# Kernel optimization log

Measured on AMD Instinct MI355X. Metric: run time of the kernel, lower is better.

The kernel has to match this reference:

```python
import jax, jax.numpy as jnp
import numpy as np

EMBED_DIM = 1024
NUM_HEADS = 16
HEAD_DIM = EMBED_DIM // NUM_HEADS


def setup_inputs() -> dict:
    key = jax.random.key(0)
    k1, k2, k3, k4, k5 = jax.random.split(key, 5)
    B, T, C = 2, 2048, EMBED_DIM
    s = 1.0 / np.sqrt(C)
    return {
        "x": jax.random.normal(k1, (B, T, C), dtype=jnp.float32),
        "W_qkv": jax.random.normal(k2, (C, 3 * C), dtype=jnp.float32) * s,
        "b_qkv": jnp.zeros((3 * C,), dtype=jnp.float32),
        "W_out": jax.random.normal(k3, (C, C), dtype=jnp.float32) * s,
        "b_out": jnp.zeros((C,), dtype=jnp.float32),
    }


def reference(x, W_qkv, b_qkv, W_out, b_out):
    B, T, C = x.shape
    H, D = NUM_HEADS, HEAD_DIM
    qkv = x @ W_qkv + b_qkv                       # [B, T, 3C]
    q, k, v = jnp.split(qkv, 3, axis=-1)
    # [B, H, T, D]
    q = q.reshape(B, T, H, D).transpose(0, 2, 1, 3)
    k = k.reshape(B, T, H, D).transpose(0, 2, 1, 3)
    v = v.reshape(B, T, H, D).transpose(0, 2, 1, 3)
    scores = jnp.einsum("bhqd,bhkd->bhqk", q, k) / np.sqrt(D)  # [B,H,T,T]
    causal = jnp.tril(jnp.ones((T, T), dtype=bool))
    scores = jnp.where(causal[None, None], scores, -jnp.inf)
    weights = jax.nn.softmax(scores, axis=-1)
    out = jnp.einsum("bhqk,bhkd->bhqd", weights, v)  # [B,H,T,D]
    out = out.transpose(0, 2, 1, 3).reshape(B, T, C)
    return out @ W_out + b_out
```

## Files before the change

### kernel.cpp

```cpp
#include <hip/hip_runtime.h>
#include <stdint.h>

typedef unsigned short u16t;
typedef __attribute__((ext_vector_type(8))) short bf16x8;
typedef __attribute__((ext_vector_type(4))) float f32x4;

#define DEV __device__ __forceinline__

DEV u16t f2bf(float f) {
  union { float f; unsigned u; } v; v.f = f;
  unsigned r = v.u + 0x7FFFu + ((v.u >> 16) & 1u);
  return (u16t)(r >> 16);
}

DEV unsigned cvtpk(float a, float b) {
  unsigned r;
  asm("v_cvt_pk_bf16_f32 %0, %1, %2" : "=v"(r) : "v"(a), "v"(b));
  return r;
}

DEV void glds16(const void* g, void* l) {
  __builtin_amdgcn_global_load_lds((const __attribute__((address_space(1))) void*)g,
                                   (__attribute__((address_space(3))) void*)l, 16, 0, 0);
}

__global__ __launch_bounds__(256) void k_cast_x(const float* __restrict__ x,
                                                u16t* __restrict__ xb, int n) {
  int i = (blockIdx.x * 256 + threadIdx.x) * 8;
  if (i >= n) return;
  const float4* p = (const float4*)(x + i);
  float4 a = p[0], b = p[1];
  union { u16t h[8]; int4 v; } o;
  o.h[0] = f2bf(a.x); o.h[1] = f2bf(a.y); o.h[2] = f2bf(a.z); o.h[3] = f2bf(a.w);
  o.h[4] = f2bf(b.x); o.h[5] = f2bf(b.y); o.h[6] = f2bf(b.z); o.h[7] = f2bf(b.w);
  *(int4*)(xb + i) = o.v;
}

__global__ __launch_bounds__(256) void k_transpose_cast(const float* __restrict__ src,
                                                        u16t* __restrict__ dst,
                                                        int R, int C) {
  __shared__ u16t tile[64][65];
  int c0 = blockIdx.x * 64, r0 = blockIdx.y * 64;
  int tid = threadIdx.x;
#pragma unroll
  for (int i = 0; i < 16; i++) {
    int idx = tid + i * 256;
    int r = idx >> 6, c = idx & 63;
    tile[c][r] = f2bf(src[(size_t)(r0 + r) * C + (c0 + c)]);
  }
  __syncthreads();
#pragma unroll
  for (int i = 0; i < 16; i++) {
    int idx = tid + i * 256;
    int rr = idx >> 6, cc = idx & 63;
    dst[(size_t)(c0 + rr) * R + (r0 + cc)] = tile[rr][cc];
  }
}

template <int K>
DEV void gemm_mainloop(const u16t* __restrict__ A, const u16t* __restrict__ Bt,
                       int m0, int n0, u16t* ldsA, u16t* ldsB, f32x4 acc[4][4]) {
  const int tid = threadIdx.x;
  const int lane = tid & 63;
  const int wid = tid >> 6;
  const int wm = wid >> 1, wn = wid & 1;
#pragma unroll
  for (int i = 0; i < 4; i++)
#pragma unroll
    for (int j = 0; j < 4; j++) acc[i][j] = f32x4{0.f, 0.f, 0.f, 0.f};

  char* lA = (char*)ldsA;
  char* lB = (char*)ldsB;

  for (int k0 = 0; k0 < K; k0 += 32) {
#pragma unroll
    for (int j = 0; j < 2; j++) {
      int g = wid * 64 + lane + j * 256;
      int row = g >> 2;
      int cb = (g & 3) * 16;
      glds16((const char*)(A + (size_t)(m0 + row) * K + k0) + cb,
             lA + j * 4096 + wid * 1024);
      glds16((const char*)(Bt + (size_t)(n0 + row) * K + k0) + cb,
             lB + j * 4096 + wid * 1024);
    }
    __syncthreads();
    bf16x8 af[4], bfr[4];
    const int lr = lane & 15;
    const int ko = (lane >> 4) * 8;
#pragma unroll
    for (int f = 0; f < 4; f++) {
      af[f]  = *(const bf16x8*)(ldsA + (wm * 64 + f * 16 + lr) * 32 + ko);
      bfr[f] = *(const bf16x8*)(ldsB + (wn * 64 + f * 16 + lr) * 32 + ko);
    }
#pragma unroll
    for (int i = 0; i < 4; i++)
#pragma unroll
      for (int j = 0; j < 4; j++)
        acc[i][j] = __builtin_amdgcn_mfma_f32_16x16x32_bf16(af[i], bfr[j], acc[i][j], 0, 0, 0);
    __syncthreads();
  }
}

__global__ __launch_bounds__(256) void k_gemm_qkv(const u16t* __restrict__ xb,
                                                  const u16t* __restrict__ wt,
                                                  const float* __restrict__ bias,
                                                  u16t* __restrict__ q,
                                                  u16t* __restrict__ kk,
                                                  u16t* __restrict__ vt) {
  __shared__ u16t ldsA[128 * 32];
  __shared__ u16t ldsB[128 * 32];
  __shared__ u16t ldsE[4][64 * 64];
  const int m0 = blockIdx.x * 128, n0 = blockIdx.y * 128;
  f32x4 acc[4][4];
  gemm_mainloop<1024>(xb, wt, m0, n0, ldsA, ldsB, acc);

  const int lane = threadIdx.x & 63, wid = threadIdx.x >> 6;
  const int wm = wid >> 1, wn = wid & 1;
  const int nbase = n0 + wn * 64;
  const int which = nbase >> 10;
  const int hb = (nbase & 1023) >> 6;
  const int bb = m0 >> 11;
  const int t0 = (m0 & 2047) + wm * 64;
  const int bh = bb * 16 + hb;
  u16t* eb = ldsE[wid];
#pragma unroll
  for (int fm = 0; fm < 4; fm++) {
#pragma unroll
    for (int fn = 0; fn < 4; fn++) {
      float bv = bias[nbase + fn * 16 + (lane & 15)];
#pragma unroll
      for (int i = 0; i < 4; i++) {
        int t_loc = fm * 16 + (lane >> 4) * 4 + i;
        int d_loc = fn * 16 + (lane & 15);
        float v = acc[fm][fn][i] + bv;
        if (which == 2) eb[d_loc * 64 + t_loc] = f2bf(v);
        else            eb[t_loc * 64 + d_loc] = f2bf(v);
      }
    }
  }
  asm volatile("s_waitcnt lgkmcnt(0)" ::: "memory");
  u16t* dst;
  size_t base, rowstride;
  if (which == 2) { dst = vt; base = (size_t)bh * 64 * 2048 + t0; rowstride = 2048; }
  else { dst = (which == 0) ? q : kk; base = ((size_t)bh * 2048 + t0) * 64; rowstride = 64; }
#pragma unroll
  for (int it = 0; it < 8; it++) {
    int g = it * 64 + lane;
    int r = g >> 3;
    int ce = (g & 7) * 8;
    *(int4*)(dst + base + (size_t)r * rowstride + ce) = *(const int4*)(eb + r * 64 + ce);
  }
}

__global__ __launch_bounds__(128) void k_attn(const u16t* __restrict__ q,
                                              const u16t* __restrict__ kk,
                                              const u16t* __restrict__ vt,
                                              u16t* __restrict__ attn) {
  __shared__ u16t ldsK[2][64 * 64];
  __shared__ u16t ldsV[2][64 * 64];
  __shared__ u16t ldsP[2][16 * 64];
  const int p = blockIdx.x;
  const int t_lo = p, t_hi = 63 - p;
  const int lo_tiles = (t_lo >> 1) + 1;
  const int hi_tiles = (t_hi >> 1) + 1;
  const int bh = blockIdx.y;
  const int tid = threadIdx.x;
  const int lane = tid & 63, wid = tid >> 6;
  const int lr = lane & 15, lg = lane >> 4;
  const size_t hbase = (size_t)bh * 2048 * 64;
  const size_t vbase = (size_t)bh * 64 * 2048;
  const float NINF = -__builtin_inff();
  const float CEXP = 0.1803368801111204f;

  bf16x8 qlo[2], qhi[2];
  {
    const u16t* qp  = q + hbase + (size_t)(t_lo * 32 + wid * 16 + lr) * 64 + lg * 8;
    const u16t* qp2 = q + hbase + (size_t)(t_hi * 32 + wid * 16 + lr) * 64 + lg * 8;
#pragma unroll
    for (int ks = 0; ks < 2; ks++) {
      qlo[ks] = *(const bf16x8*)(qp + ks * 32);
      qhi[ks] = *(const bf16x8*)(qp2 + ks * 32);
    }
  }

  f32x4 olo[4], ohi[4];
#pragma unroll
  for (int i = 0; i < 4; i++) {
    olo[i] = f32x4{0.f, 0.f, 0.f, 0.f};
    ohi[i] = f32x4{0.f, 0.f, 0.f, 0.f};
  }
  float mlo = NINF, llo = 0.f, mhi = NINF, lhi = 0.f;

  u16t* pb = ldsP[wid];

  auto stage = [&](int buf, int kt) {
#pragma unroll
    for (int j = 0; j < 4; j++) {
      int g = j * 128 + tid;
      int r = g >> 3;
      int cb = (g & 7) * 16;
      int sc = cb ^ ((r & 7) << 4);
      glds16((const char*)(kk + hbase + (size_t)(kt * 64 + r) * 64) + sc,
             (char*)ldsK[buf] + j * 2048 + wid * 1024);
      glds16((const char*)(vt + vbase + (size_t)r * 2048 + kt * 64) + sc,
             (char*)ldsV[buf] + j * 2048 + wid * 1024);
    }
  };

  auto compute = [&](int buf, bool diag, int moff, const bf16x8* qf, f32x4* o,
                     float& m_run, float& l_run) {
    const char* K = (const char*)ldsK[buf];
    const char* V = (const char*)ldsV[buf];
    float sv[4][4];
    __builtin_amdgcn_s_setprio(1);
#pragma unroll
    for (int f = 0; f < 4; f++) {
      f32x4 s = f32x4{0.f, 0.f, 0.f, 0.f};
#pragma unroll
      for (int ks = 0; ks < 2; ks++) {
        int row = f * 16 + lr;
        int cb = ks * 64 + lg * 16;
        bf16x8 kf = *(const bf16x8*)(K + row * 128 + (cb ^ ((row & 7) << 4)));
        s = __builtin_amdgcn_mfma_f32_16x16x32_bf16(kf, qf[ks], s, 0, 0, 0);
      }
#pragma unroll
      for (int i = 0; i < 4; i++) sv[f][i] = s[i];
    }
    __builtin_amdgcn_s_setprio(0);
    if (diag) {
      int qr = moff + wid * 16 + lr;
#pragma unroll
      for (int f = 0; f < 4; f++)
#pragma unroll
        for (int i = 0; i < 4; i++)
          if (f * 16 + lg * 4 + i > qr) sv[f][i] = NINF;
    }
    float m0a = fmaxf(fmaxf(sv[0][0], sv[0][1]), fmaxf(sv[0][2], sv[0][3]));
    float m1a = fmaxf(fmaxf(sv[1][0], sv[1][1]), fmaxf(sv[1][2], sv[1][3]));
    float m2a = fmaxf(fmaxf(sv[2][0], sv[2][1]), fmaxf(sv[2][2], sv[2][3]));
    float m3a = fmaxf(fmaxf(sv[3][0], sv[3][1]), fmaxf(sv[3][2], sv[3][3]));
    float mx = fmaxf(fmaxf(m0a, m1a), fmaxf(m2a, m3a));
    mx = fmaxf(mx, __shfl_xor(mx, 16));
    mx = fmaxf(mx, __shfl_xor(mx, 32));
    if (!__all(mx <= m_run + 8.0f)) {
      float mnew = fmaxf(m_run, mx);
      float al = exp2f((m_run - mnew) * CEXP);
      m_run = mnew;
      l_run *= al;
#pragma unroll
      for (int df = 0; df < 4; df++)
#pragma unroll
        for (int i = 0; i < 4; i++) o[df][i] *= al;
    }
    const float nmc = -m_run * CEXP;
    float ps[4][4];
    float fs[4];
#pragma unroll
    for (int f = 0; f < 4; f++) {
#pragma unroll
      for (int i = 0; i < 4; i++)
        ps[f][i] = exp2f(__builtin_fmaf(sv[f][i], CEXP, nmc));
      fs[f] = (ps[f][0] + ps[f][1]) + (ps[f][2] + ps[f][3]);
    }
    float ssum = (fs[0] + fs[1]) + (fs[2] + fs[3]);
    ssum += __shfl_xor(ssum, 16);
    ssum += __shfl_xor(ssum, 32);
    l_run += ssum;
#pragma unroll
    for (int f = 0; f < 4; f++) {
      union { unsigned u[2]; uint2 v; } pk;
      pk.u[0] = cvtpk(ps[f][0], ps[f][1]);
      pk.u[1] = cvtpk(ps[f][2], ps[f][3]);
      int cby = (f * 32 + lg * 8) ^ ((lr & 7) << 4);
      *(uint2*)((char*)pb + lr * 128 + cby) = pk.v;
    }
    asm volatile("s_waitcnt lgkmcnt(0)" ::: "memory");
    __builtin_amdgcn_s_setprio(1);
#pragma unroll
    for (int ks = 0; ks < 2; ks++) {
      int cb = ks * 64 + lg * 16;
      bf16x8 pf = *(const bf16x8*)((const char*)pb + lr * 128 + (cb ^ ((lr & 7) << 4)));
#pragma unroll
      for (int df = 0; df < 4; df++) {
        int vrow = df * 16 + lr;
        bf16x8 vf = *(const bf16x8*)(V + vrow * 128 + (cb ^ ((vrow & 7) << 4)));
        o[df] = __builtin_amdgcn_mfma_f32_16x16x32_bf16(vf, pf, o[df], 0, 0, 0);
      }
    }
    __builtin_amdgcn_s_setprio(0);
  };

  stage(0, 0);
  __syncthreads();
  for (int kt = 0; kt < hi_tiles; kt++) {
    int cur = kt & 1;
    if (kt + 1 < hi_tiles) stage(cur ^ 1, kt + 1);
    compute(cur, kt == (t_hi >> 1), (t_hi & 1) << 5, qhi, ohi, mhi, lhi);
    if (kt < lo_tiles) compute(cur, kt == (t_lo >> 1), (t_lo & 1) << 5, qlo, olo, mlo, llo);
    __syncthreads();
  }

  const int bb = bh >> 4, h = bh & 15;
  auto epi = [&](int qt, const f32x4* o, float l_run) {
    float rinv = 1.0f / l_run;
    int t = qt * 32 + wid * 16 + lr;
    size_t rowb = ((size_t)bb * 2048 + t) * 1024 + h * 64;
#pragma unroll
    for (int df = 0; df < 4; df++) {
      union { unsigned u[2]; uint2 v; } pk;
      pk.u[0] = cvtpk(o[df][0] * rinv, o[df][1] * rinv);
      pk.u[1] = cvtpk(o[df][2] * rinv, o[df][3] * rinv);
      *(uint2*)(attn + rowb + df * 16 + lg * 4) = pk.v;
    }
  };
  epi(t_lo, olo, llo);
  epi(t_hi, ohi, lhi);
}

__global__ __launch_bounds__(256) void k_gemm_out(const u16t* __restrict__ attn,
                                                  const u16t* __restrict__ wt,
                                                  const float* __restrict__ bias,
                                                  float* __restrict__ out) {
  __shared__ u16t ldsA[128 * 32];
  __shared__ u16t ldsB[128 * 32];
  const int m0 = blockIdx.x * 128, n0 = blockIdx.y * 128;
  f32x4 acc[4][4];
  gemm_mainloop<1024>(attn, wt, m0, n0, ldsA, ldsB, acc);

  const int lane = threadIdx.x & 63, wid = threadIdx.x >> 6;
  const int wm = wid >> 1, wn = wid & 1;
#pragma unroll
  for (int fm = 0; fm < 4; fm++) {
    int row = m0 + wm * 64 + fm * 16 + (lane >> 4) * 4;
#pragma unroll
    for (int fn = 0; fn < 4; fn++) {
      int col = n0 + wn * 64 + fn * 16 + (lane & 15);
      float bv = bias[col];
#pragma unroll
      for (int i = 0; i < 4; i++)
        out[(size_t)(row + i) * 1024 + col] = acc[fm][fn][i] + bv;
    }
  }
}

extern "C" void kernel_launch(void* const* d_in, const int* in_sizes, int n_in,
                              void* d_out, int out_size, void* d_ws, size_t ws_size,
                              hipStream_t stream) {
  const float* x     = (const float*)d_in[0];
  const float* W_qkv = (const float*)d_in[1];
  const float* b_qkv = (const float*)d_in[2];
  const float* W_out = (const float*)d_in[3];
  const float* b_out = (const float*)d_in[4];
  float* out = (float*)d_out;

  char* ws = (char*)d_ws;
  u16t* xb    = (u16t*)(ws);
  u16t* wqkvT = (u16t*)(ws + 8388608);
  u16t* woutT = (u16t*)(ws + 14680064);
  u16t* qb    = (u16t*)(ws + 16777216);
  u16t* kb    = (u16t*)(ws + 25165824);
  u16t* vtb   = (u16t*)(ws + 33554432);
  u16t* attnb = (u16t*)(ws + 41943040);

  k_cast_x<<<2048, 256, 0, stream>>>(x, xb, 4194304);
  k_transpose_cast<<<dim3(48, 16), 256, 0, stream>>>(W_qkv, wqkvT, 1024, 3072);
  k_transpose_cast<<<dim3(16, 16), 256, 0, stream>>>(W_out, woutT, 1024, 1024);
  k_gemm_qkv<<<dim3(32, 24), 256, 0, stream>>>(xb, wqkvT, b_qkv, qb, kb, vtb);
  k_attn<<<dim3(32, 32), 128, 0, stream>>>(qb, kb, vtb, attnb);
  k_gemm_out<<<dim3(32, 8), 256, 0, stream>>>(attnb, woutT, b_out, out);
}
```

Measured before the change: 133.3 us.

## Replace paired lo/hi query tiles with one 64-row tile per 4-wave block

The attention kernel previously gave each 2-wave block two 32-row query tiles (one early, one late) for causal load balancing, sharing each K/V tile load. Now each 4-wave block owns a single 64-row query tile, walks its own causal prefix of K/V tiles, and processes the largest tiles first via reversed block index. This removes the dual accumulator state and the second compute pass per tile, which lowers register pressure and raises waves per block. In exchange the blocks have uneven amounts of work and each K/V tile is reused by 64 query rows instead of 64 rows split across two tiles at different positions.

New measurement: 144.9 us. 8.7% more time.

```diff
diff --git a/kernel.cpp b/kernel.cpp
--- a/kernel.cpp
+++ b/kernel.cpp
@@ -152,18 +152,16 @@
   }
 }
 
-__global__ __launch_bounds__(128) void k_attn(const u16t* __restrict__ q,
-                                              const u16t* __restrict__ kk,
-                                              const u16t* __restrict__ vt,
-                                              u16t* __restrict__ attn) {
+__global__ __launch_bounds__(256, 4) void k_attn(const u16t* __restrict__ q,
+                                                 const u16t* __restrict__ kk,
+                                                 const u16t* __restrict__ vt,
+                                                 u16t* __restrict__ attn) {
   __shared__ u16t ldsK[2][64 * 64];
   __shared__ u16t ldsV[2][64 * 64];
-  __shared__ u16t ldsP[2][16 * 64];
-  const int p = blockIdx.x;
-  const int t_lo = p, t_hi = 63 - p;
-  const int lo_tiles = (t_lo >> 1) + 1;
-  const int hi_tiles = (t_hi >> 1) + 1;
+  __shared__ u16t ldsP[4][16 * 64];
+  const int qt = 31 - blockIdx.x;
   const int bh = blockIdx.y;
+  const int ntiles = qt + 1;
   const int tid = threadIdx.x;
   const int lane = tid & 63, wid = tid >> 6;
   const int lr = lane & 15, lg = lane >> 4;
@@ -172,43 +170,35 @@
   const float NINF = -__builtin_inff();
   const float CEXP = 0.1803368801111204f;
 
-  bf16x8 qlo[2], qhi[2];
+  bf16x8 qf[2];
   {
-    const u16t* qp  = q + hbase + (size_t)(t_lo * 32 + wid * 16 + lr) * 64 + lg * 8;
-    const u16t* qp2 = q + hbase + (size_t)(t_hi * 32 + wid * 16 + lr) * 64 + lg * 8;
-#pragma unroll
-    for (int ks = 0; ks < 2; ks++) {
-      qlo[ks] = *(const bf16x8*)(qp + ks * 32);
-      qhi[ks] = *(const bf16x8*)(qp2 + ks * 32);
-    }
-  }
-
-  f32x4 olo[4], ohi[4];
-#pragma unroll
-  for (int i = 0; i < 4; i++) {
-    olo[i] = f32x4{0.f, 0.f, 0.f, 0.f};
-    ohi[i] = f32x4{0.f, 0.f, 0.f, 0.f};
-  }
-  float mlo = NINF, llo = 0.f, mhi = NINF, lhi = 0.f;
+    const u16t* qp = q + hbase + (size_t)(qt * 64 + wid * 16 + lr) * 64 + lg * 8;
+    qf[0] = *(const bf16x8*)(qp);
+    qf[1] = *(const bf16x8*)(qp + 32);
+  }
+
+  f32x4 o[4];
+#pragma unroll
+  for (int i = 0; i < 4; i++) o[i] = f32x4{0.f, 0.f, 0.f, 0.f};
+  float m_run = NINF, l_run = 0.f;
 
   u16t* pb = ldsP[wid];
 
   auto stage = [&](int buf, int kt) {
 #pragma unroll
-    for (int j = 0; j < 4; j++) {
-      int g = j * 128 + tid;
+    for (int j = 0; j < 2; j++) {
+      int g = j * 256 + tid;
       int r = g >> 3;
       int cb = (g & 7) * 16;
       int sc = cb ^ ((r & 7) << 4);
       glds16((const char*)(kk + hbase + (size_t)(kt * 64 + r) * 64) + sc,
-             (char*)ldsK[buf] + j * 2048 + wid * 1024);
+             (char*)ldsK[buf] + j * 4096 + wid * 1024);
       glds16((const char*)(vt + vbase + (size_t)r * 2048 + kt * 64) + sc,
-             (char*)ldsV[buf] + j * 2048 + wid * 1024);
+             (char*)ldsV[buf] + j * 4096 + wid * 1024);
     }
   };
 
-  auto compute = [&](int buf, bool diag, int moff, const bf16x8* qf, f32x4* o,
-                     float& m_run, float& l_run) {
+  auto compute = [&](int buf, bool diag) {
     const char* K = (const char*)ldsK[buf];
     const char* V = (const char*)ldsV[buf];
     float sv[4][4];
@@ -228,7 +218,7 @@
     }
     __builtin_amdgcn_s_setprio(0);
     if (diag) {
-      int qr = moff + wid * 16 + lr;
+      int qr = wid * 16 + lr;
 #pragma unroll
       for (int f = 0; f < 4; f++)
 #pragma unroll
@@ -292,29 +282,24 @@
 
   stage(0, 0);
   __syncthreads();
-  for (int kt = 0; kt < hi_tiles; kt++) {
+  for (int kt = 0; kt < ntiles; kt++) {
     int cur = kt & 1;
-    if (kt + 1 < hi_tiles) stage(cur ^ 1, kt + 1);
-    compute(cur, kt == (t_hi >> 1), (t_hi & 1) << 5, qhi, ohi, mhi, lhi);
-    if (kt < lo_tiles) compute(cur, kt == (t_lo >> 1), (t_lo & 1) << 5, qlo, olo, mlo, llo);
+    if (kt + 1 < ntiles) stage(cur ^ 1, kt + 1);
+    compute(cur, kt == ntiles - 1);
     __syncthreads();
   }
 
   const int bb = bh >> 4, h = bh & 15;
-  auto epi = [&](int qt, const f32x4* o, float l_run) {
-    float rinv = 1.0f / l_run;
-    int t = qt * 32 + wid * 16 + lr;
-    size_t rowb = ((size_t)bb * 2048 + t) * 1024 + h * 64;
-#pragma unroll
-    for (int df = 0; df < 4; df++) {
-      union { unsigned u[2]; uint2 v; } pk;
-      pk.u[0] = cvtpk(o[df][0] * rinv, o[df][1] * rinv);
-      pk.u[1] = cvtpk(o[df][2] * rinv, o[df][3] * rinv);
-      *(uint2*)(attn + rowb + df * 16 + lg * 4) = pk.v;
-    }
-  };
-  epi(t_lo, olo, llo);
-  epi(t_hi, ohi, lhi);
+  float rinv = 1.0f / l_run;
+  int t = qt * 64 + wid * 16 + lr;
+  size_t rowb = ((size_t)bb * 2048 + t) * 1024 + h * 64;
+#pragma unroll
+  for (int df = 0; df < 4; df++) {
+    union { unsigned u[2]; uint2 v; } pk;
+    pk.u[0] = cvtpk(o[df][0] * rinv, o[df][1] * rinv);
+    pk.u[1] = cvtpk(o[df][2] * rinv, o[df][3] * rinv);
+    *(uint2*)(attn + rowb + df * 16 + lg * 4) = pk.v;
+  }
 }
 
 __global__ __launch_bounds__(256) void k_gemm_out(const u16t* __restrict__ attn,
@@ -366,6 +351,6 @@
   k_transpose_cast<<<dim3(48, 16), 256, 0, stream>>>(W_qkv, wqkvT, 1024, 3072);
   k_transpose_cast<<<dim3(16, 16), 256, 0, stream>>>(W_out, woutT, 1024, 1024);
   k_gemm_qkv<<<dim3(32, 24), 256, 0, stream>>>(xb, wqkvT, b_qkv, qb, kb, vtb);
-  k_attn<<<dim3(32, 32), 128, 0, stream>>>(qb, kb, vtb, attnb);
+  k_attn<<<dim3(32, 32), 256, 0, stream>>>(qb, kb, vtb, attnb);
   k_gemm_out<<<dim3(32, 8), 256, 0, stream>>>(attnb, woutT, b_out, out);
 }
```
